# Performance work log

Hardware: AMD Instinct MI355X
Metric: run time of the kernel (lower is better)

The kernel has to match this reference:

```python
import jax, jax.numpy as jnp
import numpy as np

HEADS = 4
DIM_HEAD = 64
SCALE = 8.0
EPS = 1e-5  # fp32 branch of the original LayerNorm


def setup_inputs() -> dict:
    key = jax.random.key(0)
    k1, k2, k3 = jax.random.split(key, 3)
    B, C, F, H, W = 2, 256, 4, 32, 32
    inner = HEADS * DIM_HEAD  # 256
    x = jax.random.normal(k1, (B, C, F, H, W), dtype=jnp.float32)
    gamma = jnp.ones((1, C, 1, 1, 1), dtype=jnp.float32)
    w_qkv = jax.random.normal(k2, (3 * inner, C), dtype=jnp.float32) * 0.05
    w_out = jax.random.normal(k3, (C, inner), dtype=jnp.float32) * 0.05
    return {"x": x, "gamma": gamma, "w_qkv": w_qkv, "w_out": w_out}


def _l2norm(t):
    return t / jnp.sqrt(jnp.sum(t * t, axis=-1, keepdims=True) + 1e-12)


def reference(x, gamma, w_qkv, w_out):
    B, C, F, H, W = x.shape
    N = F * H * W
    inner = HEADS * DIM_HEAD
    residual = x

    # channel LayerNorm (biased variance over dim=1)
    mean = jnp.mean(x, axis=1, keepdims=True)
    var = jnp.mean((x - mean) ** 2, axis=1, keepdims=True)
    xn = (x - mean) / jnp.sqrt(var + EPS) * gamma

    # 1x1x1 conv == channel matmul; flatten spatial dims to sequence
    xn_flat = xn.reshape(B, C, N)                      # [B, C, N]
    qkv = jnp.einsum('oc,bcn->bon', w_qkv, xn_flat)    # [B, 3*inner, N]
    qkv = qkv.reshape(B, 3, HEADS, DIM_HEAD, N)        # chunk then split heads
    qkv = jnp.transpose(qkv, (1, 0, 2, 4, 3))          # [3, B, h, N, d]
    q, k, v = qkv[0], qkv[1], qkv[2]

    q = _l2norm(q)
    k = _l2norm(k)

    sim = jnp.einsum('bhid,bhjd->bhij', q, k) * SCALE  # [B, h, N, N]
    attn = jax.nn.softmax(sim, axis=-1)
    out = jnp.einsum('bhij,bhjd->bhid', attn, v)       # [B, h, N, d]

    # 'b h n d -> b (h d) n' then 1x1x1 out conv
    out = jnp.transpose(out, (0, 1, 3, 2)).reshape(B, inner, N)
    out = jnp.einsum('oi,bin->bon', w_out, out).reshape(B, C, F, H, W)
    return out + residual
```

## Files before the change

### kernel.cpp

```cpp
#include <hip/hip_runtime.h>

#define BATCH 2
#define CCH   256
#define NSEQ  4096
#define NH    4
#define DH    64
#define INNER 256

typedef __attribute__((ext_vector_type(8))) __bf16 bf16x8;
typedef __attribute__((ext_vector_type(4))) float f32x4;
typedef __attribute__((ext_vector_type(8))) unsigned short u16x8;
typedef __attribute__((ext_vector_type(4))) unsigned short u16x4;

#define GLD16(gsrc, ldst)                                                     \
  __builtin_amdgcn_global_load_lds(                                           \
      (const __attribute__((address_space(1))) unsigned int*)(const void*)(gsrc), \
      (__attribute__((address_space(3))) unsigned int*)(void*)(ldst), 16, 0, 0)

static __device__ __forceinline__ unsigned short f2bfr(float f) {
  union { float f; unsigned u; } v; v.f = f;
  return (unsigned short)((v.u + 0x8000u) >> 16);
}
static __device__ __forceinline__ unsigned pack2(float f0, float f1) {
  union { float f; unsigned u; } a, b; a.f = f0; b.f = f1;
  return __builtin_amdgcn_perm(b.u + 0x8000u, a.u + 0x8000u, 0x07060302u);
}
static __device__ __forceinline__ float bf2f(unsigned short u) {
  union { unsigned u; float f; } v; v.u = ((unsigned)u) << 16;
  return v.f;
}
static __device__ __forceinline__ bf16x8 ldb(const unsigned short* p) {
  return *(const bf16x8*)p;
}
static __device__ __forceinline__ f32x4 mm(bf16x8 a, bf16x8 b, f32x4 c) {
  return __builtin_amdgcn_mfma_f32_16x16x32_bf16(a, b, c, 0, 0, 0);
}

__global__ __launch_bounds__(256) void k_lncvt(const float* __restrict__ x,
                                               const float* __restrict__ gamma,
                                               unsigned short* __restrict__ xn,
                                               const float* __restrict__ wq,
                                               const float* __restrict__ wo,
                                               unsigned short* __restrict__ wqb,
                                               unsigned short* __restrict__ wob) {
  int blk = blockIdx.x;
  if (blk >= 256) {
    int t = (blk - 256) * 256 + threadIdx.x;
    int e = t * 4;
    if (e < 768 * 256) {
      float4 v = *(const float4*)(wq + e);
      u16x4 pk = { f2bfr(v.x), f2bfr(v.y), f2bfr(v.z), f2bfr(v.w) };
      *(u16x4*)(wqb + e) = pk;
    } else {
      int e2 = e - 768 * 256;
      float4 v = *(const float4*)(wo + e2);
      u16x4 pk = { f2bfr(v.x), f2bfr(v.y), f2bfr(v.z), f2bfr(v.w) };
      *(u16x4*)(wob + e2) = pk;
    }
    return;
  }
  int b  = blk >> 7;
  int n0 = (blk & 127) * 32;
  int t  = threadIdx.x;
  int nl = t & 31;
  int cg = t >> 5;
  int n  = n0 + nl;
  const float* xp = x + ((size_t)(b * CCH + cg * 32)) * NSEQ + n;
  float vals[32];
  float s = 0.f, s2 = 0.f;
#pragma unroll
  for (int j = 0; j < 32; j++) {
    float v = xp[(size_t)j * NSEQ];
    vals[j] = v; s += v; s2 += v * v;
  }
  __shared__ float rs[8][32], rs2[8][32];
  rs[cg][nl] = s; rs2[cg][nl] = s2;
  __syncthreads();
  float S = 0.f, S2 = 0.f;
#pragma unroll
  for (int g = 0; g < 8; g++) { S += rs[g][nl]; S2 += rs2[g][nl]; }
  float mean = S * (1.f / 256.f);
  float var  = S2 * (1.f / 256.f) - mean * mean;
  float rstd = rsqrtf(var + 1e-5f);
  unsigned short* dst = xn + ((size_t)b * NSEQ + n) * CCH + cg * 32;
#pragma unroll
  for (int j0 = 0; j0 < 32; j0 += 8) {
    u16x8 pk;
#pragma unroll
    for (int j = 0; j < 8; j++)
      pk[j] = f2bfr((vals[j0 + j] - mean) * rstd * gamma[cg * 32 + j0 + j]);
    *(u16x8*)(dst + j0) = pk;
  }
}

__global__ __launch_bounds__(256) void k_qkv(const unsigned short* __restrict__ wqb,
                                             const unsigned short* __restrict__ xn,
                                             unsigned short* __restrict__ qkv,
                                             unsigned short* __restrict__ qt,
                                             unsigned short* __restrict__ ktb) {
  int n0 = blockIdx.x * 64;
  int oi = blockIdx.y;
  int o0 = oi * 64;
  int b  = blockIdx.z;
  __shared__ unsigned short Al[64 * 128];
  __shared__ unsigned short Bl[64 * 128];
  int t = threadIdx.x;
  int lane = t & 63, w = t >> 6;
  int c = lane & 15, quad = lane >> 4;
  int wm = w >> 1, wn = w & 1;
  f32x4 acc[2][2] = {};
  int lr = lane >> 4;
  int lchk = lane & 15;
  const unsigned short* apg = wqb + (size_t)o0 * CCH;
  const unsigned short* bpg = xn + ((size_t)b * NSEQ + n0) * CCH;
  for (int kt = 0; kt < 2; kt++) {
    if (kt) __syncthreads();
#pragma unroll
    for (int q = 0; q < 4; q++) {
      int r = w * 16 + q * 4 + lr;
      int srcoff = r * CCH + kt * 128 + ((lchk ^ (r & 7)) * 8);
      unsigned short* ldst = (w * 16 + q * 4) * 128 + (unsigned short*)0;
      GLD16(apg + srcoff, Al + (size_t)(w * 16 + q * 4) * 128);
      GLD16(bpg + srcoff, Bl + (size_t)(w * 16 + q * 4) * 128);
      (void)ldst;
    }
    __syncthreads();
#pragma unroll
    for (int ks = 0; ks < 4; ks++) {
      int ra0 = wm * 32 + c, ra1 = ra0 + 16;
      int rb0 = wn * 32 + c, rb1 = rb0 + 16;
      bf16x8 a0 = ldb(&Al[ra0 * 128 + (((ks * 4 + quad) ^ (ra0 & 7)) * 8)]);
      bf16x8 a1 = ldb(&Al[ra1 * 128 + (((ks * 4 + quad) ^ (ra1 & 7)) * 8)]);
      bf16x8 b0 = ldb(&Bl[rb0 * 128 + (((ks * 4 + quad) ^ (rb0 & 7)) * 8)]);
      bf16x8 b1 = ldb(&Bl[rb1 * 128 + (((ks * 4 + quad) ^ (rb1 & 7)) * 8)]);
      acc[0][0] = mm(a0, b0, acc[0][0]);
      acc[0][1] = mm(a0, b1, acc[0][1]);
      acc[1][0] = mm(a1, b0, acc[1][0]);
      acc[1][1] = mm(a1, b1, acc[1][1]);
    }
  }
  if (oi < 8) {
    float* sq = (float*)Al;
    float s0 = 0.f, s1 = 0.f;
#pragma unroll
    for (int i = 0; i < 2; i++)
#pragma unroll
      for (int rr = 0; rr < 4; rr++) {
        s0 += acc[i][0][rr] * acc[i][0][rr];
        s1 += acc[i][1][rr] * acc[i][1][rr];
      }
    s0 += __shfl_xor(s0, 16); s0 += __shfl_xor(s0, 32);
    s1 += __shfl_xor(s1, 16); s1 += __shfl_xor(s1, 32);
    __syncthreads();
    if (quad == 0) {
      sq[wm * 64 + wn * 32 + c]      = s0;
      sq[wm * 64 + wn * 32 + 16 + c] = s1;
    }
    __syncthreads();
    float r0 = rsqrtf(sq[wn * 32 + c]      + sq[64 + wn * 32 + c]      + 1e-12f);
    float r1 = rsqrtf(sq[wn * 32 + 16 + c] + sq[64 + wn * 32 + 16 + c] + 1e-12f);
    if (oi < 4) { r0 *= 11.541560327111707f; r1 *= 11.541560327111707f; }
    int h = oi & 3;
    unsigned short* base = (oi < 4 ? qt : ktb) + ((size_t)(b * NH + h) * NSEQ) * DH;
#pragma unroll
    for (int i = 0; i < 2; i++)
#pragma unroll
      for (int j = 0; j < 2; j++) {
        float rsc = j ? r1 : r0;
        int n = n0 + wn * 32 + j * 16 + c;
        int d = wm * 32 + i * 16 + quad * 4;
        uint2 pk = { pack2(acc[i][j][0] * rsc, acc[i][j][1] * rsc),
                     pack2(acc[i][j][2] * rsc, acc[i][j][3] * rsc) };
        *(uint2*)(base + (size_t)n * DH + d) = pk;
      }
  } else {
#pragma unroll
    for (int i = 0; i < 2; i++)
#pragma unroll
      for (int j = 0; j < 2; j++)
#pragma unroll
        for (int rr = 0; rr < 4; rr++) {
          int o = o0 + wm * 32 + i * 16 + quad * 4 + rr;
          int n = n0 + wn * 32 + j * 16 + c;
          qkv[((size_t)b * 768 + o) * NSEQ + n] = f2bfr(acc[i][j][rr]);
        }
  }
}

__global__ __launch_bounds__(256, 6) void k_attn(
    const unsigned short* __restrict__ qt,
    const unsigned short* __restrict__ ktb,
    const unsigned short* __restrict__ qkv,
    unsigned short* __restrict__ ao,
    unsigned short* __restrict__ opart,
    float* __restrict__ lpart,
    int S, int kvlen) {
  int i0 = blockIdx.x * 64;
  int h  = blockIdx.y;
  int bz = blockIdx.z;
  int b  = bz / S, s = bz % S;
  __shared__ unsigned short Kl[64 * 64];
  __shared__ unsigned short Vl[64 * 64];
  __shared__ unsigned short Pl[64 * 72];
  int t = threadIdx.x;
  int lane = t & 63, w = t >> 6;
  int c = lane & 15, quad = lane >> 4;
  int r = t >> 2, seg = (t & 3) * 16;

  const unsigned short* qbase = qt  + ((size_t)(b * NH + h) * NSEQ) * DH;
  const unsigned short* kbase = ktb + ((size_t)(b * NH + h) * NSEQ) * DH;
  const unsigned short* vbase = qkv + ((size_t)b * 768 + 512 + h * 64) * NSEQ;

  {
    const unsigned short* p = qbase + (size_t)(i0 + r) * DH + seg;
    *(u16x8*)&Pl[r * 72 + seg]     = *(const u16x8*)p;
    *(u16x8*)&Pl[r * 72 + seg + 8] = *(const u16x8*)(p + 8);
  }
  __syncthreads();
  bf16x8 qf0 = ldb(&Pl[(w * 16 + c) * 72 + quad * 8]);
  bf16x8 qf1 = ldb(&Pl[(w * 16 + c) * 72 + 32 + quad * 8]);
  __syncthreads();

  u16x8 onesu;
#pragma unroll
  for (int j = 0; j < 8; j++) onesu[j] = 0x3F80;
  bf16x8 ones = *(bf16x8*)&onesu;

  f32x4 acc[4] = {};
  f32x4 accl = {};

  int lr = lane >> 3, lc = lane & 7;
  int ssw = (lc ^ lr) * 8;
  const unsigned short* kp = kbase + (size_t)(s * kvlen + w * 16 + lr) * DH + ssw;
  const unsigned short* vp = vbase + (size_t)(w * 16 + lr) * NSEQ + s * kvlen + ssw;
  unsigned short* kl0 = Kl + (w * 16)     * 64;
  unsigned short* kl1 = Kl + (w * 16 + 8) * 64;
  unsigned short* vl0 = Vl + (w * 16)     * 64;
  unsigned short* vl1 = Vl + (w * 16 + 8) * 64;
  int sw0 = (quad ^ (c & 7)) * 8;
  int sw1 = sw0 ^ 32;

  for (int it = 0; it < kvlen / 64; it++) {
    GLD16(kp,             kl0);
    GLD16(kp + 8 * DH,    kl1);
    GLD16(vp,             vl0);
    GLD16(vp + 8 * NSEQ,  vl1);
    kp += 64 * DH; vp += 64;
    __syncthreads();

#pragma unroll
    for (int jt = 0; jt < 4; jt++) {
      f32x4 z = {};
      z = mm(ldb(&Kl[(jt * 16 + c) * 64 + sw0]), qf0, z);
      z = mm(ldb(&Kl[(jt * 16 + c) * 64 + sw1]), qf1, z);
      uint2 pk = { pack2(exp2f(z[0]), exp2f(z[1])),
                   pack2(exp2f(z[2]), exp2f(z[3])) };
      *(uint2*)&Pl[(w * 16 + c) * 72 + jt * 16 + quad * 4] = pk;
    }
    bf16x8 pa0 = ldb(&Pl[(w * 16 + c) * 72 + quad * 8]);
    bf16x8 pa1 = ldb(&Pl[(w * 16 + c) * 72 + 32 + quad * 8]);
#pragma unroll
    for (int dt = 0; dt < 4; dt++) {
      acc[dt] = mm(pa0, ldb(&Vl[(dt * 16 + c) * 64 + sw0]), acc[dt]);
      acc[dt] = mm(pa1, ldb(&Vl[(dt * 16 + c) * 64 + sw1]), acc[dt]);
    }
    accl = mm(pa0, ones, accl);
    accl = mm(pa1, ones, accl);
    __syncthreads();
  }

  if (S > 1) {
    size_t rb = ((size_t)(b * NH + h) * S + s) * NSEQ + i0 + w * 16;
    if (c == 0) {
#pragma unroll
      for (int rr = 0; rr < 4; rr++) lpart[rb + quad * 4 + rr] = accl[rr];
    }
#pragma unroll
    for (int rr = 0; rr < 4; rr++)
#pragma unroll
      for (int dt = 0; dt < 4; dt++)
        opart[(rb + quad * 4 + rr) * 64 + dt * 16 + c] = f2bfr(acc[dt][rr]);
  } else {
#pragma unroll
    for (int rr = 0; rr < 4; rr++) {
      float inv = 1.f / accl[rr];
      int i = i0 + w * 16 + quad * 4 + rr;
#pragma unroll
      for (int dt = 0; dt < 4; dt++)
        ao[((size_t)b * NSEQ + i) * INNER + h * 64 + dt * 16 + c] =
            f2bfr(acc[dt][rr] * inv);
    }
  }
}

__global__ __launch_bounds__(256) void k_merge(
    const unsigned short* __restrict__ opart,
    const float* __restrict__ lpart,
    unsigned short* __restrict__ ao, int S) {
  int t = blockIdx.x * 256 + threadIdx.x;
  int row = t >> 2;
  int dseg = (t & 3) * 16;
  int b = row >> 14, rem = row & 16383;
  int h = rem >> 12, i = rem & 4095;

  float l = 0.f;
  float o[16];
#pragma unroll
  for (int j = 0; j < 16; j++) o[j] = 0.f;
  for (int s = 0; s < S; s++) {
    size_t rb = ((size_t)(b * NH + h) * S + s) * NSEQ + i;
    l += lpart[rb];
    const unsigned short* p = opart + rb * 64 + dseg;
    u16x8 v0 = *(const u16x8*)p;
    u16x8 v1 = *(const u16x8*)(p + 8);
#pragma unroll
    for (int j = 0; j < 8; j++) {
      o[j]     += bf2f(v0[j]);
      o[8 + j] += bf2f(v1[j]);
    }
  }
  float inv = 1.f / l;
  unsigned short* dst = ao + ((size_t)b * NSEQ + i) * INNER + h * 64 + dseg;
  uint4 pk0 = { pack2(o[0] * inv, o[1] * inv),  pack2(o[2] * inv, o[3] * inv),
                pack2(o[4] * inv, o[5] * inv),  pack2(o[6] * inv, o[7] * inv) };
  uint4 pk1 = { pack2(o[8] * inv, o[9] * inv),  pack2(o[10] * inv, o[11] * inv),
                pack2(o[12] * inv, o[13] * inv),pack2(o[14] * inv, o[15] * inv) };
  *(uint4*)dst = pk0;
  *(uint4*)(dst + 8) = pk1;
}

__global__ __launch_bounds__(256) void k_out(const unsigned short* __restrict__ wob,
                                             const unsigned short* __restrict__ ao,
                                             const float* __restrict__ x,
                                             float* __restrict__ out) {
  int n0 = blockIdx.x * 64;
  int o0 = blockIdx.y * 64;
  int b  = blockIdx.z;
  __shared__ unsigned short Al[64 * 128];
  __shared__ unsigned short Bl[64 * 128];
  int t = threadIdx.x;
  int lane = t & 63, w = t >> 6;
  int c = lane & 15, quad = lane >> 4;
  int wm = w >> 1, wn = w & 1;
  f32x4 acc[2][2] = {};
  int lr = lane >> 4;
  int lchk = lane & 15;
  const unsigned short* apg = wob + (size_t)o0 * INNER;
  const unsigned short* bpg = ao + ((size_t)b * NSEQ + n0) * INNER;
  for (int kt = 0; kt < 2; kt++) {
    if (kt) __syncthreads();
#pragma unroll
    for (int q = 0; q < 4; q++) {
      int r = w * 16 + q * 4 + lr;
      int srcoff = r * INNER + kt * 128 + ((lchk ^ (r & 7)) * 8);
      GLD16(apg + srcoff, Al + (size_t)(w * 16 + q * 4) * 128);
      GLD16(bpg + srcoff, Bl + (size_t)(w * 16 + q * 4) * 128);
    }
    __syncthreads();
#pragma unroll
    for (int ks = 0; ks < 4; ks++) {
      int ra0 = wm * 32 + c, ra1 = ra0 + 16;
      int rb0 = wn * 32 + c, rb1 = rb0 + 16;
      bf16x8 a0 = ldb(&Al[ra0 * 128 + (((ks * 4 + quad) ^ (ra0 & 7)) * 8)]);
      bf16x8 a1 = ldb(&Al[ra1 * 128 + (((ks * 4 + quad) ^ (ra1 & 7)) * 8)]);
      bf16x8 b0 = ldb(&Bl[rb0 * 128 + (((ks * 4 + quad) ^ (rb0 & 7)) * 8)]);
      bf16x8 b1 = ldb(&Bl[rb1 * 128 + (((ks * 4 + quad) ^ (rb1 & 7)) * 8)]);
      acc[0][0] = mm(a0, b0, acc[0][0]);
      acc[0][1] = mm(a0, b1, acc[0][1]);
      acc[1][0] = mm(a1, b0, acc[1][0]);
      acc[1][1] = mm(a1, b1, acc[1][1]);
    }
  }
#pragma unroll
  for (int i = 0; i < 2; i++)
#pragma unroll
    for (int j = 0; j < 2; j++)
#pragma unroll
      for (int rr = 0; rr < 4; rr++) {
        int o = o0 + wm * 32 + i * 16 + quad * 4 + rr;
        int n = n0 + wn * 32 + j * 16 + c;
        size_t idx = ((size_t)b * CCH + o) * NSEQ + n;
        out[idx] = acc[i][j][rr] + x[idx];
      }
}

extern "C" void kernel_launch(void* const* d_in, const int* in_sizes, int n_in,
                              void* d_out, int out_size, void* d_ws, size_t ws_size,
                              hipStream_t stream) {
  const float* x     = (const float*)d_in[0];
  const float* gamma = (const float*)d_in[1];
  const float* wq    = (const float*)d_in[2];
  const float* wo    = (const float*)d_in[3];
  float* out = (float*)d_out;

  const size_t MB = 1u << 20;
  char* ws = (char*)d_ws;
  unsigned short* ao  = (unsigned short*)ws;
  unsigned short* xn  = (unsigned short*)(ws + 4 * MB);
  unsigned short* qkv = (unsigned short*)(ws + 8 * MB);
  unsigned short* wqb = (unsigned short*)(ws + 20 * MB);
  unsigned short* wob = (unsigned short*)(ws + 20 * MB + 512 * 1024);
  unsigned short* qt  = (unsigned short*)(ws + 21 * MB);
  unsigned short* ktb = (unsigned short*)(ws + 25 * MB);
  unsigned short* opart = (unsigned short*)(ws + 29 * MB);
  int S;
  if (ws_size >= 48 * MB) S = 4;
  else if (ws_size >= 39 * MB) S = 2;
  else S = 1;
  size_t opart_bytes = (size_t)S * BATCH * NH * NSEQ * DH * 2;
  float* lpart = (float*)(ws + 29 * MB + opart_bytes);
  int kvlen = NSEQ / S;

  k_lncvt<<<dim3(512),         256, 0, stream>>>(x, gamma, xn, wq, wo, wqb, wob);
  k_qkv  <<<dim3(64, 12, 2),   256, 0, stream>>>(wqb, xn, qkv, qt, ktb);
  k_attn <<<dim3(64, 4, 2 * S),256, 0, stream>>>(qt, ktb, qkv, ao, opart,
                                                 lpart, S, kvlen);
  if (S > 1)
    k_merge<<<dim3(512), 256, 0, stream>>>(opart, lpart, ao, S);
  k_out  <<<dim3(64, 4, 2),    256, 0, stream>>>(wob, ao, x, out);
}
```

Baseline: 148.7 us.

## Double attention query tile per block and fuse split-KV merge into output projection

The attention kernel now handles 128 query rows per block, two 16-row fragments per wave. Each K/V tile loaded into LDS is therefore reused for twice as many queries, and Q is loaded directly from global memory into registers. The separate merge kernel is removed: the output-projection kernel sums the split-KV partials, normalizes them and writes the swizzled B tile into LDS itself, which saves a launch and the intermediate round trip. The trade-offs are higher register pressure (launch bounds occupancy lowered from 6 to 4), half as many attention blocks, and each of the four output-channel blocks redundantly re-reading and re-merging the same partials.

After: 148.6 us. Within noise of the previous version (-0.1%).

```diff
diff --git a/kernel.cpp b/kernel.cpp
--- a/kernel.cpp
+++ b/kernel.cpp
@@ -119,10 +119,8 @@
     for (int q = 0; q < 4; q++) {
       int r = w * 16 + q * 4 + lr;
       int srcoff = r * CCH + kt * 128 + ((lchk ^ (r & 7)) * 8);
-      unsigned short* ldst = (w * 16 + q * 4) * 128 + (unsigned short*)0;
       GLD16(apg + srcoff, Al + (size_t)(w * 16 + q * 4) * 128);
       GLD16(bpg + srcoff, Bl + (size_t)(w * 16 + q * 4) * 128);
-      (void)ldst;
     }
     __syncthreads();
 #pragma unroll
@@ -187,152 +185,117 @@
   }
 }
 
-__global__ __launch_bounds__(256, 6) void k_attn(
+__global__ __launch_bounds__(256, 4) void k_attn(
     const unsigned short* __restrict__ qt,
     const unsigned short* __restrict__ ktb,
     const unsigned short* __restrict__ qkv,
-    unsigned short* __restrict__ ao,
     unsigned short* __restrict__ opart,
     float* __restrict__ lpart,
     int S, int kvlen) {
-  int i0 = blockIdx.x * 64;
+  int i0 = blockIdx.x * 128;
   int h  = blockIdx.y;
   int bz = blockIdx.z;
   int b  = bz / S, s = bz % S;
   __shared__ unsigned short Kl[64 * 64];
   __shared__ unsigned short Vl[64 * 64];
-  __shared__ unsigned short Pl[64 * 72];
+  __shared__ unsigned short Pl[128 * 64];
   int t = threadIdx.x;
   int lane = t & 63, w = t >> 6;
   int c = lane & 15, quad = lane >> 4;
-  int r = t >> 2, seg = (t & 3) * 16;
 
   const unsigned short* qbase = qt  + ((size_t)(b * NH + h) * NSEQ) * DH;
   const unsigned short* kbase = ktb + ((size_t)(b * NH + h) * NSEQ) * DH;
   const unsigned short* vbase = qkv + ((size_t)b * 768 + 512 + h * 64) * NSEQ;
 
-  {
-    const unsigned short* p = qbase + (size_t)(i0 + r) * DH + seg;
-    *(u16x8*)&Pl[r * 72 + seg]     = *(const u16x8*)p;
-    *(u16x8*)&Pl[r * 72 + seg + 8] = *(const u16x8*)(p + 8);
-  }
-  __syncthreads();
-  bf16x8 qf0 = ldb(&Pl[(w * 16 + c) * 72 + quad * 8]);
-  bf16x8 qf1 = ldb(&Pl[(w * 16 + c) * 72 + 32 + quad * 8]);
-  __syncthreads();
+  int rlo = w * 32 + c, rhi = rlo + 16;
+  const unsigned short* qlo = qbase + (size_t)(i0 + rlo) * DH + quad * 8;
+  const unsigned short* qhi = qlo + 16 * DH;
+  bf16x8 qlo0 = ldb(qlo), qlo1 = ldb(qlo + 32);
+  bf16x8 qhi0 = ldb(qhi), qhi1 = ldb(qhi + 32);
 
   u16x8 onesu;
 #pragma unroll
   for (int j = 0; j < 8; j++) onesu[j] = 0x3F80;
   bf16x8 ones = *(bf16x8*)&onesu;
 
-  f32x4 acc[4] = {};
-  f32x4 accl = {};
-
-  int lr = lane >> 3, lc = lane & 7;
-  int ssw = (lc ^ lr) * 8;
-  const unsigned short* kp = kbase + (size_t)(s * kvlen + w * 16 + lr) * DH + ssw;
-  const unsigned short* vp = vbase + (size_t)(w * 16 + lr) * NSEQ + s * kvlen + ssw;
+  f32x4 acclo[4] = {}, acchi[4] = {};
+  f32x4 accllo = {}, acclhi = {};
+
+  int slr = lane >> 3, slc = lane & 7;
+  int ssw = (slc ^ slr) * 8;
+  const unsigned short* kp = kbase + (size_t)(s * kvlen + w * 16 + slr) * DH + ssw;
+  const unsigned short* vp = vbase + (size_t)(w * 16 + slr) * NSEQ + s * kvlen + ssw;
   unsigned short* kl0 = Kl + (w * 16)     * 64;
   unsigned short* kl1 = Kl + (w * 16 + 8) * 64;
   unsigned short* vl0 = Vl + (w * 16)     * 64;
   unsigned short* vl1 = Vl + (w * 16 + 8) * 64;
   int sw0 = (quad ^ (c & 7)) * 8;
   int sw1 = sw0 ^ 32;
+  int r7 = rlo & 7;
 
   for (int it = 0; it < kvlen / 64; it++) {
-    GLD16(kp,             kl0);
-    GLD16(kp + 8 * DH,    kl1);
-    GLD16(vp,             vl0);
-    GLD16(vp + 8 * NSEQ,  vl1);
+    GLD16(kp,            kl0);
+    GLD16(kp + 8 * DH,   kl1);
+    GLD16(vp,            vl0);
+    GLD16(vp + 8 * NSEQ, vl1);
     kp += 64 * DH; vp += 64;
     __syncthreads();
 
 #pragma unroll
     for (int jt = 0; jt < 4; jt++) {
-      f32x4 z = {};
-      z = mm(ldb(&Kl[(jt * 16 + c) * 64 + sw0]), qf0, z);
-      z = mm(ldb(&Kl[(jt * 16 + c) * 64 + sw1]), qf1, z);
-      uint2 pk = { pack2(exp2f(z[0]), exp2f(z[1])),
-                   pack2(exp2f(z[2]), exp2f(z[3])) };
-      *(uint2*)&Pl[(w * 16 + c) * 72 + jt * 16 + quad * 4] = pk;
-    }
-    bf16x8 pa0 = ldb(&Pl[(w * 16 + c) * 72 + quad * 8]);
-    bf16x8 pa1 = ldb(&Pl[(w * 16 + c) * 72 + 32 + quad * 8]);
+      bf16x8 k0 = ldb(&Kl[(jt * 16 + c) * 64 + sw0]);
+      bf16x8 k1 = ldb(&Kl[(jt * 16 + c) * 64 + sw1]);
+      f32x4 zl = {}; zl = mm(k0, qlo0, zl); zl = mm(k1, qlo1, zl);
+      f32x4 zh = {}; zh = mm(k0, qhi0, zh); zh = mm(k1, qhi1, zh);
+      int cj = jt * 2 + (quad >> 1);
+      int sub = (quad & 1) * 4;
+      uint2 pkl = { pack2(exp2f(zl[0]), exp2f(zl[1])),
+                    pack2(exp2f(zl[2]), exp2f(zl[3])) };
+      *(uint2*)&Pl[rlo * 64 + ((cj ^ r7) * 8) + sub] = pkl;
+      uint2 pkh = { pack2(exp2f(zh[0]), exp2f(zh[1])),
+                    pack2(exp2f(zh[2]), exp2f(zh[3])) };
+      *(uint2*)&Pl[rhi * 64 + ((cj ^ r7) * 8) + sub] = pkh;
+    }
+    bf16x8 plo0 = ldb(&Pl[rlo * 64 + ((quad ^ r7) * 8)]);
+    bf16x8 plo1 = ldb(&Pl[rlo * 64 + (((quad + 4) ^ r7) * 8)]);
+    bf16x8 phi0 = ldb(&Pl[rhi * 64 + ((quad ^ r7) * 8)]);
+    bf16x8 phi1 = ldb(&Pl[rhi * 64 + (((quad + 4) ^ r7) * 8)]);
 #pragma unroll
     for (int dt = 0; dt < 4; dt++) {
-      acc[dt] = mm(pa0, ldb(&Vl[(dt * 16 + c) * 64 + sw0]), acc[dt]);
-      acc[dt] = mm(pa1, ldb(&Vl[(dt * 16 + c) * 64 + sw1]), acc[dt]);
-    }
-    accl = mm(pa0, ones, accl);
-    accl = mm(pa1, ones, accl);
-    __syncthreads();
-  }
-
-  if (S > 1) {
-    size_t rb = ((size_t)(b * NH + h) * S + s) * NSEQ + i0 + w * 16;
-    if (c == 0) {
-#pragma unroll
-      for (int rr = 0; rr < 4; rr++) lpart[rb + quad * 4 + rr] = accl[rr];
-    }
-#pragma unroll
-    for (int rr = 0; rr < 4; rr++)
-#pragma unroll
-      for (int dt = 0; dt < 4; dt++)
-        opart[(rb + quad * 4 + rr) * 64 + dt * 16 + c] = f2bfr(acc[dt][rr]);
-  } else {
+      bf16x8 v0 = ldb(&Vl[(dt * 16 + c) * 64 + sw0]);
+      bf16x8 v1 = ldb(&Vl[(dt * 16 + c) * 64 + sw1]);
+      acclo[dt] = mm(plo0, v0, acclo[dt]);
+      acclo[dt] = mm(plo1, v1, acclo[dt]);
+      acchi[dt] = mm(phi0, v0, acchi[dt]);
+      acchi[dt] = mm(phi1, v1, acchi[dt]);
+    }
+    accllo = mm(plo0, ones, accllo); accllo = mm(plo1, ones, accllo);
+    acclhi = mm(phi0, ones, acclhi); acclhi = mm(phi1, ones, acclhi);
+    __syncthreads();
+  }
+
+  size_t rb = ((size_t)(b * NH + h) * S + s) * NSEQ + i0 + w * 32;
+  if (c == 0) {
 #pragma unroll
     for (int rr = 0; rr < 4; rr++) {
-      float inv = 1.f / accl[rr];
-      int i = i0 + w * 16 + quad * 4 + rr;
-#pragma unroll
-      for (int dt = 0; dt < 4; dt++)
-        ao[((size_t)b * NSEQ + i) * INNER + h * 64 + dt * 16 + c] =
-            f2bfr(acc[dt][rr] * inv);
-    }
-  }
-}
-
-__global__ __launch_bounds__(256) void k_merge(
-    const unsigned short* __restrict__ opart,
-    const float* __restrict__ lpart,
-    unsigned short* __restrict__ ao, int S) {
-  int t = blockIdx.x * 256 + threadIdx.x;
-  int row = t >> 2;
-  int dseg = (t & 3) * 16;
-  int b = row >> 14, rem = row & 16383;
-  int h = rem >> 12, i = rem & 4095;
-
-  float l = 0.f;
-  float o[16];
-#pragma unroll
-  for (int j = 0; j < 16; j++) o[j] = 0.f;
-  for (int s = 0; s < S; s++) {
-    size_t rb = ((size_t)(b * NH + h) * S + s) * NSEQ + i;
-    l += lpart[rb];
-    const unsigned short* p = opart + rb * 64 + dseg;
-    u16x8 v0 = *(const u16x8*)p;
-    u16x8 v1 = *(const u16x8*)(p + 8);
-#pragma unroll
-    for (int j = 0; j < 8; j++) {
-      o[j]     += bf2f(v0[j]);
-      o[8 + j] += bf2f(v1[j]);
-    }
-  }
-  float inv = 1.f / l;
-  unsigned short* dst = ao + ((size_t)b * NSEQ + i) * INNER + h * 64 + dseg;
-  uint4 pk0 = { pack2(o[0] * inv, o[1] * inv),  pack2(o[2] * inv, o[3] * inv),
-                pack2(o[4] * inv, o[5] * inv),  pack2(o[6] * inv, o[7] * inv) };
-  uint4 pk1 = { pack2(o[8] * inv, o[9] * inv),  pack2(o[10] * inv, o[11] * inv),
-                pack2(o[12] * inv, o[13] * inv),pack2(o[14] * inv, o[15] * inv) };
-  *(uint4*)dst = pk0;
-  *(uint4*)(dst + 8) = pk1;
+      lpart[rb + quad * 4 + rr]      = accllo[rr];
+      lpart[rb + 16 + quad * 4 + rr] = acclhi[rr];
+    }
+  }
+#pragma unroll
+  for (int rr = 0; rr < 4; rr++)
+#pragma unroll
+    for (int dt = 0; dt < 4; dt++) {
+      opart[(rb + quad * 4 + rr) * 64 + dt * 16 + c]      = f2bfr(acclo[dt][rr]);
+      opart[(rb + 16 + quad * 4 + rr) * 64 + dt * 16 + c] = f2bfr(acchi[dt][rr]);
+    }
 }
 
 __global__ __launch_bounds__(256) void k_out(const unsigned short* __restrict__ wob,
-                                             const unsigned short* __restrict__ ao,
+                                             const unsigned short* __restrict__ opart,
+                                             const float* __restrict__ lpart,
                                              const float* __restrict__ x,
-                                             float* __restrict__ out) {
+                                             float* __restrict__ out, int S) {
   int n0 = blockIdx.x * 64;
   int o0 = blockIdx.y * 64;
   int b  = blockIdx.z;
@@ -346,7 +309,8 @@
   int lr = lane >> 4;
   int lchk = lane & 15;
   const unsigned short* apg = wob + (size_t)o0 * INNER;
-  const unsigned short* bpg = ao + ((size_t)b * NSEQ + n0) * INNER;
+  int br = t >> 2;
+  int n  = n0 + br;
   for (int kt = 0; kt < 2; kt++) {
     if (kt) __syncthreads();
 #pragma unroll
@@ -354,7 +318,34 @@
       int r = w * 16 + q * 4 + lr;
       int srcoff = r * INNER + kt * 128 + ((lchk ^ (r & 7)) * 8);
       GLD16(apg + srcoff, Al + (size_t)(w * 16 + q * 4) * 128);
-      GLD16(bpg + srcoff, Bl + (size_t)(w * 16 + q * 4) * 128);
+    }
+    float linv[2];
+#pragma unroll
+    for (int hh = 0; hh < 2; hh++) {
+      int h = kt * 2 + hh;
+      float l = 0.f;
+      for (int s = 0; s < S; s++)
+        l += lpart[((size_t)(b * NH + h) * S + s) * NSEQ + n];
+      linv[hh] = 1.f / l;
+    }
+#pragma unroll
+    for (int q = 0; q < 4; q++) {
+      int cj = (t & 3) + 4 * q;
+      int hh = cj >> 3;
+      int h  = kt * 2 + hh;
+      int d  = (cj & 7) * 8;
+      float o[8] = {};
+      for (int s = 0; s < S; s++) {
+        const unsigned short* p =
+            opart + (((size_t)(b * NH + h) * S + s) * NSEQ + n) * 64 + d;
+        u16x8 v = *(const u16x8*)p;
+#pragma unroll
+        for (int j = 0; j < 8; j++) o[j] += bf2f(v[j]);
+      }
+      float iv = linv[hh];
+      uint4 pk = { pack2(o[0] * iv, o[1] * iv), pack2(o[2] * iv, o[3] * iv),
+                   pack2(o[4] * iv, o[5] * iv), pack2(o[6] * iv, o[7] * iv) };
+      *(uint4*)&Bl[br * 128 + ((cj ^ (br & 7)) * 8)] = pk;
     }
     __syncthreads();
 #pragma unroll
@@ -378,8 +369,8 @@
 #pragma unroll
       for (int rr = 0; rr < 4; rr++) {
         int o = o0 + wm * 32 + i * 16 + quad * 4 + rr;
-        int n = n0 + wn * 32 + j * 16 + c;
-        size_t idx = ((size_t)b * CCH + o) * NSEQ + n;
+        int nn = n0 + wn * 32 + j * 16 + c;
+        size_t idx = ((size_t)b * CCH + o) * NSEQ + nn;
         out[idx] = acc[i][j][rr] + x[idx];
       }
 }
@@ -395,27 +386,24 @@
 
   const size_t MB = 1u << 20;
   char* ws = (char*)d_ws;
-  unsigned short* ao  = (unsigned short*)ws;
-  unsigned short* xn  = (unsigned short*)(ws + 4 * MB);
-  unsigned short* qkv = (unsigned short*)(ws + 8 * MB);
-  unsigned short* wqb = (unsigned short*)(ws + 20 * MB);
-  unsigned short* wob = (unsigned short*)(ws + 20 * MB + 512 * 1024);
-  unsigned short* qt  = (unsigned short*)(ws + 21 * MB);
-  unsigned short* ktb = (unsigned short*)(ws + 25 * MB);
-  unsigned short* opart = (unsigned short*)(ws + 29 * MB);
+  unsigned short* xn  = (unsigned short*)ws;
+  unsigned short* qkv = (unsigned short*)(ws + 4 * MB);
+  unsigned short* wqb = (unsigned short*)(ws + 16 * MB);
+  unsigned short* wob = (unsigned short*)(ws + 16 * MB + 512 * 1024);
+  unsigned short* qt  = (unsigned short*)(ws + 17 * MB);
+  unsigned short* ktb = (unsigned short*)(ws + 21 * MB);
+  unsigned short* opart = (unsigned short*)(ws + 25 * MB);
   int S;
-  if (ws_size >= 48 * MB) S = 4;
-  else if (ws_size >= 39 * MB) S = 2;
+  if (ws_size >= 45 * MB) S = 4;
+  else if (ws_size >= 36 * MB) S = 2;
   else S = 1;
   size_t opart_bytes = (size_t)S * BATCH * NH * NSEQ * DH * 2;
-  float* lpart = (float*)(ws + 29 * MB + opart_bytes);
+  float* lpart = (float*)(ws + 25 * MB + opart_bytes);
   int kvlen = NSEQ / S;
 
-  k_lncvt<<<dim3(512),         256, 0, stream>>>(x, gamma, xn, wq, wo, wqb, wob);
-  k_qkv  <<<dim3(64, 12, 2),   256, 0, stream>>>(wqb, xn, qkv, qt, ktb);
-  k_attn <<<dim3(64, 4, 2 * S),256, 0, stream>>>(qt, ktb, qkv, ao, opart,
-                                                 lpart, S, kvlen);
-  if (S > 1)
-    k_merge<<<dim3(512), 256, 0, stream>>>(opart, lpart, ao, S);
-  k_out  <<<dim3(64, 4, 2),    256, 0, stream>>>(wob, ao, x, out);
-}
+  k_lncvt<<<dim3(512),          256, 0, stream>>>(x, gamma, xn, wq, wo, wqb, wob);
+  k_qkv  <<<dim3(64, 12, 2),    256, 0, stream>>>(wqb, xn, qkv, qt, ktb);
+  k_attn <<<dim3(32, 4, 2 * S), 256, 0, stream>>>(qt, ktb, qkv, opart,
+                                                  lpart, S, kvlen);
+  k_out  <<<dim3(64, 4, 2),     256, 0, stream>>>(wob, opart, lpart, x, out, S);
+}
```
